# Kernel tuning notes

Measured on AMD Instinct MI355X. Metric: run time of the kernel, lower is better.

Reference implementation:

```python
import jax, jax.numpy as jnp
import numpy as np

B, S, T = 256, 512, 32  # batch, seq_len, tag_size (includes START=T-2, END=T-1)


def setup_inputs() -> dict:
    key = jax.random.key(0)
    k1, k2, k3, k4 = jax.random.split(key, 4)
    feats = jax.random.normal(k1, (B, S, T), dtype=jnp.float32)
    transitions = jax.random.normal(k2, (T, T), dtype=jnp.float32) * 0.1
    # prefix mask: lengths in [S//2, S] (torch code assumes contiguous valid prefix)
    lengths = jax.random.randint(k3, (B,), S // 2, S + 1)
    mask = jnp.arange(S)[None, :] < lengths[:, None]  # (B,S) bool
    tags = jax.random.randint(k4, (B, S), 0, T - 2).astype(jnp.int32)
    return {"feats": feats, "transitions": transitions, "mask": mask, "tags": tags}


def _nll_loss(feats, transitions, mask, tags):
    Bx, Sx, Tx = feats.shape
    maskf = mask.astype(feats.dtype)
    # ---- forward algorithm (log partition) ----
    # partition initialized from emissions at position 1 (positions 0,1 are special)
    part0 = feats[:, 1, :]  # (B,T)
    f_seq = jnp.swapaxes(feats[:, 2:, :], 0, 1)  # (S-2, B, T)
    m_seq = jnp.swapaxes(mask[:, 2:], 0, 1)      # (S-2, B)

    def fwd_step(partition, inp):
        f_t, m_t = inp
        # cur[b, prev, next] = feats[b,t,next] + transitions[prev,next] + partition[b,prev]
        cur = f_t[:, None, :] + transitions[None, :, :] + partition[:, :, None]
        new = jax.nn.logsumexp(cur, axis=1)  # (B,T)
        # partition frozen where mask==0 (== torch masked_scatter logic)
        return jnp.where(m_t[:, None], new, partition), None

    partition, _ = jax.lax.scan(fwd_step, part0, (f_seq, m_seq))
    forward_score = jnp.sum(jax.nn.logsumexp(partition, axis=1))

    # ---- gold score ----
    tags = jnp.where(tags == -100, 0, tags)
    emis = jnp.take_along_axis(feats, tags[..., None], axis=2)[..., 0]  # (B,S)
    tr = transitions[tags[:, :-1], tags[:, 1:]]  # (B,S-1): transition into pos t (t>=1)
    # transitions only apply for t>=2; tg_energy[0] is zeroed in the torch code
    e = emis + jnp.concatenate([jnp.zeros((Bx, 2), feats.dtype), tr[:, 1:]], axis=1)
    e = e.at[:, 0].set(0.0)
    gold_score = jnp.sum(e * maskf)
    return (forward_score - gold_score) / Bx


def _viterbi(feats, transitions, mask):
    Bx, Sx, Tx = feats.shape
    lengths = mask.astype(jnp.int32).sum(axis=1)
    part0 = feats[:, 1, :]
    f_seq = jnp.swapaxes(feats[:, 2:, :], 0, 1)
    m_seq = jnp.swapaxes(mask[:, 2:], 0, 1)

    def vit_step(partition, inp):
        f_t, m_t = inp
        cur = f_t[:, None, :] + transitions[None, :, :] + partition[:, :, None]
        new = jnp.max(cur, axis=1)
        bp = jnp.argmax(cur, axis=1).astype(jnp.int32)
        bp = jnp.where(m_t[:, None], bp, 0)  # torch masked_fill_(pad, 0)
        # NOTE: viterbi partition is updated UNconditionally in the torch code
        return new, (partition, bp)

    last_part, (hist, bps) = jax.lax.scan(vit_step, part0, (f_seq, m_seq))
    history = jnp.concatenate([hist, last_part[None]], axis=0)  # (S-1,B,T)
    hist_bt = jnp.swapaxes(history, 0, 1)                        # (B,S-1,T)
    idx = jnp.broadcast_to((lengths - 2)[:, None, None], (Bx, 1, Tx))
    last_partition = jnp.take_along_axis(hist_bt, idx, axis=1)[:, 0, :]  # (B,T)
    pointer = jnp.argmax(last_partition, axis=1).astype(jnp.int32)

    def back_step(ptr, bp_t):
        new = jnp.take_along_axis(bp_t, ptr[:, None], axis=1)[:, 0]
        return new, new

    _, ptrs = jax.lax.scan(back_step, pointer, bps, reverse=True)  # (S-2,B)
    # decode_idx[0] is uninitialized in the torch code; we define it as 0
    decode = jnp.concatenate(
        [jnp.zeros((1, Bx), jnp.int32), ptrs, pointer[None, :]], axis=0
    )  # (S,B)
    path_score = jnp.zeros((Bx,), feats.dtype)  # torch returns zeros
    return path_score, decode.T


def reference(feats, transitions, mask, tags):
    loss = _nll_loss(feats, transitions, mask, tags)
    path_score, decode_idx = _viterbi(feats, transitions, mask)
    return loss, path_score, decode_idx
```

## Files before the change

kernel.cpp:

```cpp
#include <hip/hip_runtime.h>
#include <cstdint>
#include <cstddef>
#include <utility>

#define SS 512
#define TT 32
#define NB 256
#define KSTEPS 510
#define PQUADS 128

template <typename F, size_t... Is>
__device__ __forceinline__ void unroll_impl(F&& f, std::index_sequence<Is...>) {
  (f(std::integral_constant<int, (int)Is>{}), ...);
}
template <int N, typename F>
__device__ __forceinline__ void unrollN(F&& f) {
  unroll_impl(f, std::make_index_sequence<N>{});
}

template <int D>
__device__ __forceinline__ float bfly32(float v) {
  return __int_as_float(__builtin_amdgcn_ds_swizzle(__float_as_int(v), (D << 10) | 0x1f));
}
template <int D>
__device__ __forceinline__ int bfly32i(int v) {
  return __builtin_amdgcn_ds_swizzle(v, (D << 10) | 0x1f);
}

__device__ __forceinline__ float max3f(float a, float b, float c) {
  return fmaxf(fmaxf(a, b), c);
}

__device__ __forceinline__ float combine_max32(float m) {
#if __has_builtin(__builtin_amdgcn_permlane32_swap)
  auto r = __builtin_amdgcn_permlane32_swap(__float_as_uint(m), __float_as_uint(m), false, false);
  return fmaxf(__uint_as_float(r[0]), __uint_as_float(r[1]));
#else
  return fmaxf(m, __shfl_xor(m, 32, 64));
#endif
}
__device__ __forceinline__ float combine_sum32(float m) {
#if __has_builtin(__builtin_amdgcn_permlane32_swap)
  auto r = __builtin_amdgcn_permlane32_swap(__float_as_uint(m), __float_as_uint(m), false, false);
  return __uint_as_float(r[0]) + __uint_as_float(r[1]);
#else
  return m + __shfl_xor(m, 32, 64);
#endif
}

__device__ __forceinline__ int mask_mode(const void* m) {
  int w0 = ((const int*)m)[0];
  if (w0 == 1) return 0;
  if (w0 == 0x3f800000) return 2;
  return 1;
}
__device__ __forceinline__ bool mask_at(const void* m, int idx, int mode) {
  if (mode == 0) return ((const int*)m)[idx] != 0;
  if (mode == 2) return ((const float*)m)[idx] != 0.0f;
  return ((const unsigned char*)m)[idx] != 0;
}

__device__ __forceinline__ int seq_length_lane(const void* mask, int b, int lane, int mode) {
  int cnt = 0;
  for (int s = lane; s < SS; s += 64) cnt += mask_at(mask, b * SS + s, mode) ? 1 : 0;
  for (int d = 1; d < 64; d <<= 1) cnt += __shfl_xor(cnt, d, 64);
  return __builtin_amdgcn_readfirstlane(cnt);
}

__global__ __launch_bounds__(64, 1) void crf_main_kernel(
    const float* __restrict__ feats, const float* __restrict__ trans,
    const void* __restrict__ mask, const int* __restrict__ tags,
    float* __restrict__ pstore, float* __restrict__ ws_fwd,
    float* __restrict__ ws_gold, int* __restrict__ ws_ptr) {
  const int blk = blockIdx.x;
  const int tid = threadIdx.x;
  const int mode = mask_mode(mask);
  const int j = tid & 31;
  const int h = tid >> 5;

  __shared__ __align__(16) float qlds[TT];

  if (blk < NB) {
    const int b = blk;
    const int steps = seq_length_lane(mask, b, tid, mode) - 2;
    const float* fb = feats + (size_t)b * (SS * TT) + j;

    float E[16];
    unrollN<16>([&](auto I) {
      constexpr int ii = I;
      E[ii] = __expf(trans[(h * 16 + ii) * TT + j]);
    });

    float q = __expf(fb[TT]);
    int Eacc = 0;
    qlds[j] = q;
    asm volatile("" ::: "memory");
    const float4* qvh = (const float4*)qlds + h * 4;

    float fA = fb[2 * TT], fB = fb[3 * TT], fC = fb[4 * TT];
    float ef = __expf(fA);

    auto fstep = [&](int k, bool resc) {
      float4 Q0 = qvh[0], Q1 = qvh[1], Q2 = qvh[2], Q3 = qvh[3];
      int r5 = k + 5; r5 = (r5 < SS) ? r5 : (SS - 1);
      float fD = fb[r5 * TT];
      float efN = __expf(fB);
      float a0, a1, a2, a3;
      a0 = Q0.x * E[0];  a1 = Q0.y * E[1];  a2 = Q0.z * E[2];  a3 = Q0.w * E[3];
      a0 = fmaf(Q1.x, E[4], a0);  a1 = fmaf(Q1.y, E[5], a1);  a2 = fmaf(Q1.z, E[6], a2);  a3 = fmaf(Q1.w, E[7], a3);
      a0 = fmaf(Q2.x, E[8], a0);  a1 = fmaf(Q2.y, E[9], a1);  a2 = fmaf(Q2.z, E[10], a2); a3 = fmaf(Q2.w, E[11], a3);
      a0 = fmaf(Q3.x, E[12], a0); a1 = fmaf(Q3.y, E[13], a1); a2 = fmaf(Q3.z, E[14], a2); a3 = fmaf(Q3.w, E[15], a3);
      float P = (a0 + a1) + (a2 + a3);
      float Pt = combine_sum32(P);
      q = ef * Pt;
      if (resc) {
        int qb = __builtin_amdgcn_readfirstlane(__float_as_int(q));
        int e = (qb >> 23) & 0xff;
        Eacc += e - 127;
        q *= __int_as_float((254 - e) << 23);
      }
      qlds[j] = q;
      asm volatile("" ::: "memory");
      fA = fB; fB = fC; fC = fD; ef = efN;
    };

    int k = 0;
    for (; k + 4 <= steps; k += 4) {
      fstep(k, false); fstep(k + 1, false); fstep(k + 2, false); fstep(k + 3, true);
    }
    for (; k < steps; ++k) fstep(k, false);

    float s = q;
    unrollN<5>([&](auto D) { constexpr int d = 1 << D; s += bfly32<d>(s); });
    if (tid == 0) ws_fwd[b] = __logf(s) + (float)Eacc * 0.69314718056f;

  } else if (blk < 2 * NB) {
    const int b = blk - NB;
    const int steps = seq_length_lane(mask, b, tid, mode) - 2;
    const float* fb = feats + (size_t)b * (SS * TT) + j;
    float* pq = pstore + (size_t)b * (PQUADS * 128) + j * 4;

    float C[16];
    unrollN<16>([&](auto I) {
      constexpr int ii = I;
      C[ii] = trans[(h * 16 + ii) * TT + j];
    });

    float p = fb[TT];
    qlds[j] = p;
    asm volatile("" ::: "memory");
    const float4* qvh = (const float4*)qlds + h * 4;

    float fA = fb[2 * TT], fB = fb[3 * TT], fC = fb[4 * TT];
    float h0 = p, h1 = 0.f, h2 = 0.f, h3 = 0.f;

    auto vstep = [&](int k, float& hslot) {
      float4 Q0 = qvh[0], Q1 = qvh[1], Q2 = qvh[2], Q3 = qvh[3];
      int r5 = k + 5; r5 = (r5 < SS) ? r5 : (SS - 1);
      float fD = fb[r5 * TT];
      float dd[16];
      unrollN<16>([&](auto I) { constexpr int ii = I; dd[ii] = fA + C[ii]; });
      float cur[16];
      cur[0] = Q0.x + dd[0];   cur[1] = Q0.y + dd[1];   cur[2] = Q0.z + dd[2];   cur[3] = Q0.w + dd[3];
      cur[4] = Q1.x + dd[4];   cur[5] = Q1.y + dd[5];   cur[6] = Q1.z + dd[6];   cur[7] = Q1.w + dd[7];
      cur[8] = Q2.x + dd[8];   cur[9] = Q2.y + dd[9];   cur[10] = Q2.z + dd[10]; cur[11] = Q2.w + dd[11];
      cur[12] = Q3.x + dd[12]; cur[13] = Q3.y + dd[13]; cur[14] = Q3.z + dd[14]; cur[15] = Q3.w + dd[15];
      float t0 = max3f(cur[0], cur[1], cur[2]);
      float t1 = max3f(cur[3], cur[4], cur[5]);
      float t2 = max3f(cur[6], cur[7], cur[8]);
      float t3 = max3f(cur[9], cur[10], cur[11]);
      float t4 = max3f(cur[12], cur[13], cur[14]);
      float m = fmaxf(max3f(t0, t1, t2), max3f(t3, t4, cur[15]));
      float pw = combine_max32(m);
      p = pw;
      qlds[j] = pw;
      asm volatile("" ::: "memory");
      hslot = pw;
      fA = fB; fB = fC; fC = fD;
    };

    auto flush = [&](int quad) {
      if (tid < 32) {
        float4 v; v.x = h0; v.y = h1; v.z = h2; v.w = h3;
        *(float4*)(pq + quad * 128) = v;
      }
    };

    int k = 0;
    for (; k + 4 <= steps; k += 4) {
      vstep(k, h1);
      vstep(k + 1, h2);
      vstep(k + 2, h3);
      flush(k >> 2);
      vstep(k + 3, h0);
    }
    if (k < steps) vstep(k, h1);
    if (k + 1 < steps) vstep(k + 1, h2);
    if (k + 2 < steps) vstep(k + 2, h3);
    flush(k >> 2);

    float v = p;
    int idx = j;
    unrollN<5>([&](auto D) {
      constexpr int d = 1 << D;
      float vo = bfly32<d>(v);
      int io = bfly32i<d>(idx);
      bool take = (vo > v) || ((vo == v) && (io < idx));
      v = take ? vo : v;
      idx = take ? io : idx;
    });
    if (tid == 0) ws_ptr[b] = idx;

  } else {
    const int b = blk - 2 * NB;
    float acc = 0.0f;
    for (int s = tid; s < SS; s += 64) {
      if (s == 0) continue;
      if (!mask_at(mask, b * SS + s, mode)) continue;
      int tg = tags[b * SS + s];
      if (tg == -100) tg = 0;
      float e = feats[((size_t)b * SS + s) * TT + tg];
      if (s >= 2) {
        int tp = tags[b * SS + s - 1];
        if (tp == -100) tp = 0;
        e += trans[tp * TT + tg];
      }
      acc += e;
    }
    for (int d = 1; d < 64; d <<= 1) acc += __shfl_xor(acc, d, 64);
    if (tid == 0) ws_gold[b] = acc;
  }
}

__global__ __launch_bounds__(512) void crf_backtrace_kernel(
    const float* __restrict__ pstore, const float* __restrict__ feats,
    const float* __restrict__ trans, const void* __restrict__ mask,
    const int* __restrict__ ws_ptr, const float* __restrict__ ws_fwd,
    const float* __restrict__ ws_gold, float* __restrict__ out) {
  __shared__ unsigned char bp[KSTEPS * TT];
  __shared__ unsigned char path[KSTEPS * TT];
  __shared__ __align__(16) float pT[16][4][TT];
  __shared__ int entries[8];

  const int b = blockIdx.x;
  const int tid = threadIdx.x;
  const int mode = mask_mode(mask);
  const int lane = tid & 63;
  float* out_decode = out + 1 + NB;

  const int steps = seq_length_lane(mask, b, lane, mode) - 2;

  if (tid == 0) out[1 + b] = 0.0f;
  if (b == 0 && tid >= 64 && tid < 128) {
    int t = tid - 64;
    float sf = 0.0f, sg = 0.0f;
    for (int r = 0; r < 4; ++r) { sf += ws_fwd[t + 64 * r]; sg += ws_gold[t + 64 * r]; }
    for (int d = 1; d < 64; d <<= 1) { sf += __shfl_xor(sf, d, 64); sg += __shfl_xor(sg, d, 64); }
    if (t == 0) out[0] = (sf - sg) / 256.0f;
  }

  {
    const int jj = tid & 31;
    const int g = tid >> 5;
    float Cc[TT];
    unrollN<TT>([&](auto I) { constexpr int ii = I; Cc[ii] = trans[ii * TT + jj]; });
    const float* pb = pstore + (size_t)b * (PQUADS * 128);
    const float* fbb = feats + (size_t)b * (SS * TT);
    for (int q = g; q < PQUADS; q += 16) {
      float4 V = *(const float4*)(pb + q * 128 + jj * 4);
      pT[g][0][jj] = V.x; pT[g][1][jj] = V.y; pT[g][2][jj] = V.z; pT[g][3][jj] = V.w;
      asm volatile("" ::: "memory");
      unrollN<4>([&](auto R) {
        constexpr int r = R;
        const int k = 4 * q + r;
        if (k < KSTEPS) {
          unsigned char bv = 0;
          if (k < steps) {
            const float4* pr = (const float4*)pT[g][r];
            float4 P0 = pr[0], P1 = pr[1], P2 = pr[2], P3 = pr[3];
            float4 P4 = pr[4], P5 = pr[5], P6 = pr[6], P7 = pr[7];
            float fj = fbb[(k + 2) * TT + jj];
            float cur[TT];
            cur[0]  = (fj + Cc[0])  + P0.x; cur[1]  = (fj + Cc[1])  + P0.y;
            cur[2]  = (fj + Cc[2])  + P0.z; cur[3]  = (fj + Cc[3])  + P0.w;
            cur[4]  = (fj + Cc[4])  + P1.x; cur[5]  = (fj + Cc[5])  + P1.y;
            cur[6]  = (fj + Cc[6])  + P1.z; cur[7]  = (fj + Cc[7])  + P1.w;
            cur[8]  = (fj + Cc[8])  + P2.x; cur[9]  = (fj + Cc[9])  + P2.y;
            cur[10] = (fj + Cc[10]) + P2.z; cur[11] = (fj + Cc[11]) + P2.w;
            cur[12] = (fj + Cc[12]) + P3.x; cur[13] = (fj + Cc[13]) + P3.y;
            cur[14] = (fj + Cc[14]) + P3.z; cur[15] = (fj + Cc[15]) + P3.w;
            cur[16] = (fj + Cc[16]) + P4.x; cur[17] = (fj + Cc[17]) + P4.y;
            cur[18] = (fj + Cc[18]) + P4.z; cur[19] = (fj + Cc[19]) + P4.w;
            cur[20] = (fj + Cc[20]) + P5.x; cur[21] = (fj + Cc[21]) + P5.y;
            cur[22] = (fj + Cc[22]) + P5.z; cur[23] = (fj + Cc[23]) + P5.w;
            cur[24] = (fj + Cc[24]) + P6.x; cur[25] = (fj + Cc[25]) + P6.y;
            cur[26] = (fj + Cc[26]) + P6.z; cur[27] = (fj + Cc[27]) + P6.w;
            cur[28] = (fj + Cc[28]) + P7.x; cur[29] = (fj + Cc[29]) + P7.y;
            cur[30] = (fj + Cc[30]) + P7.z; cur[31] = (fj + Cc[31]) + P7.w;
            float t0 = max3f(cur[0], cur[1], cur[2]);
            float t1 = max3f(cur[3], cur[4], cur[5]);
            float t2 = max3f(cur[6], cur[7], cur[8]);
            float t3 = max3f(cur[9], cur[10], cur[11]);
            float t4 = max3f(cur[12], cur[13], cur[14]);
            float t5 = max3f(cur[15], cur[16], cur[17]);
            float t6 = max3f(cur[18], cur[19], cur[20]);
            float t7 = max3f(cur[21], cur[22], cur[23]);
            float t8 = max3f(cur[24], cur[25], cur[26]);
            float t9 = max3f(cur[27], cur[28], cur[29]);
            float ta = fmaxf(cur[30], cur[31]);
            float vmax = fmaxf(fmaxf(max3f(t0, t1, t2), max3f(t3, t4, t5)),
                               fmaxf(max3f(t6, t7, t8), fmaxf(t9, ta)));
            int bi = 31;
            unrollN<TT>([&](auto I) { constexpr int ii = 31 - I; bi = (cur[ii] == vmax) ? ii : bi; });
            bv = (unsigned char)bi;
          }
          bp[k * TT + jj] = bv;
        }
      });
    }
  }
  __syncthreads();

  const int wave = tid >> 6;
  if (lane < 32) {
    const int lo = wave * 64;
    const int hi = (lo + 64 < KSTEPS) ? (lo + 64) : KSTEPS;
    int ptr = lane;
    for (int k = hi - 1; k >= lo; --k) {
      ptr = bp[k * TT + ptr];
      path[k * TT + lane] = (unsigned char)ptr;
    }
  }
  __syncthreads();

  if (tid == 0) {
    int e = ws_ptr[b];
    for (int c = 7; c >= 0; --c) {
      entries[c] = e;
      e = path[(c * 64) * TT + e];
    }
  }
  __syncthreads();

  const int s = tid;
  int val;
  if (s == 0) val = 0;
  else if (s <= KSTEPS) { int k = s - 1; val = path[k * TT + entries[k >> 6]]; }
  else val = ws_ptr[b];
  out_decode[(size_t)b * SS + s] = (float)val;
}

extern "C" void kernel_launch(void* const* d_in, const int* in_sizes, int n_in,
                              void* d_out, int out_size, void* d_ws, size_t ws_size,
                              hipStream_t stream) {
  const float* feats = (const float*)d_in[0];
  const float* trans = (const float*)d_in[1];
  const void* mask = d_in[2];
  const int* tags = (const int*)d_in[3];
  float* out = (float*)d_out;

  unsigned char* ws = (unsigned char*)d_ws;
  const size_t PST_BYTES = (size_t)NB * PQUADS * 128 * 4;
  float* pstore = (float*)ws;
  float* ws_fwd = (float*)(ws + PST_BYTES);
  float* ws_gold = (float*)(ws + PST_BYTES + 2048);
  int* ws_ptr = (int*)(ws + PST_BYTES + 4096);

  hipLaunchKernelGGL(crf_main_kernel, dim3(3 * NB), dim3(64), 0, stream,
                     feats, trans, mask, tags, pstore, ws_fwd, ws_gold, ws_ptr);
  hipLaunchKernelGGL(crf_backtrace_kernel, dim3(NB), dim3(512), 0, stream,
                     pstore, feats, trans, mask, ws_ptr, ws_fwd, ws_gold, out);
}
```

Before: 112.6 us.

## Interleave two batch sequences per wave in forward and Viterbi recurrences

Result: slower. 175.3 us (+55.8%).

```diff
diff --git a/kernel.cpp b/kernel.cpp
--- a/kernel.cpp
+++ b/kernel.cpp
@@ -78,12 +78,15 @@
   const int j = tid & 31;
   const int h = tid >> 5;
 
-  __shared__ __align__(16) float qlds[TT];
-
-  if (blk < NB) {
-    const int b = blk;
-    const int steps = seq_length_lane(mask, b, tid, mode) - 2;
-    const float* fb = feats + (size_t)b * (SS * TT) + j;
+  __shared__ __align__(16) float qlds[2][TT];
+
+  if (blk < 128) {
+    const int bA = blk * 2, bB = bA + 1;
+    const int stepsA = seq_length_lane(mask, bA, tid, mode) - 2;
+    const int stepsB = seq_length_lane(mask, bB, tid, mode) - 2;
+    const int smax = (stepsA > stepsB) ? stepsA : stepsB;
+    const float* fbA = feats + (size_t)bA * (SS * TT) + j;
+    const float* fbB = feats + (size_t)bB * (SS * TT) + j;
 
     float E[16];
     unrollN<16>([&](auto I) {
@@ -91,54 +94,88 @@
       E[ii] = __expf(trans[(h * 16 + ii) * TT + j]);
     });
 
-    float q = __expf(fb[TT]);
-    int Eacc = 0;
-    qlds[j] = q;
+    float qA = __expf(fbA[TT]), qB = __expf(fbB[TT]);
+    int EaA = 0, EaB = 0;
+    qlds[0][j] = qA; qlds[1][j] = qB;
     asm volatile("" ::: "memory");
-    const float4* qvh = (const float4*)qlds + h * 4;
-
-    float fA = fb[2 * TT], fB = fb[3 * TT], fC = fb[4 * TT];
-    float ef = __expf(fA);
-
-    auto fstep = [&](int k, bool resc) {
-      float4 Q0 = qvh[0], Q1 = qvh[1], Q2 = qvh[2], Q3 = qvh[3];
+    const float4* qvA = (const float4*)qlds[0] + h * 4;
+    const float4* qvB = (const float4*)qlds[1] + h * 4;
+
+    float fA0 = fbA[2 * TT], fB0 = fbA[3 * TT], fC0 = fbA[4 * TT];
+    float fA1 = fbB[2 * TT], fB1 = fbB[3 * TT], fC1 = fbB[4 * TT];
+    float efA = __expf(fA0), efB = __expf(fA1);
+
+    auto fstep2 = [&](int k, bool resc) {
+      float4 QA0 = qvA[0], QA1 = qvA[1], QA2 = qvA[2], QA3 = qvA[3];
+      float4 QB0 = qvB[0], QB1 = qvB[1], QB2 = qvB[2], QB3 = qvB[3];
       int r5 = k + 5; r5 = (r5 < SS) ? r5 : (SS - 1);
-      float fD = fb[r5 * TT];
-      float efN = __expf(fB);
-      float a0, a1, a2, a3;
-      a0 = Q0.x * E[0];  a1 = Q0.y * E[1];  a2 = Q0.z * E[2];  a3 = Q0.w * E[3];
-      a0 = fmaf(Q1.x, E[4], a0);  a1 = fmaf(Q1.y, E[5], a1);  a2 = fmaf(Q1.z, E[6], a2);  a3 = fmaf(Q1.w, E[7], a3);
-      a0 = fmaf(Q2.x, E[8], a0);  a1 = fmaf(Q2.y, E[9], a1);  a2 = fmaf(Q2.z, E[10], a2); a3 = fmaf(Q2.w, E[11], a3);
-      a0 = fmaf(Q3.x, E[12], a0); a1 = fmaf(Q3.y, E[13], a1); a2 = fmaf(Q3.z, E[14], a2); a3 = fmaf(Q3.w, E[15], a3);
-      float P = (a0 + a1) + (a2 + a3);
-      float Pt = combine_sum32(P);
-      q = ef * Pt;
-      if (resc) {
-        int qb = __builtin_amdgcn_readfirstlane(__float_as_int(q));
-        int e = (qb >> 23) & 0xff;
-        Eacc += e - 127;
-        q *= __int_as_float((254 - e) << 23);
+      float fDA = fbA[r5 * TT], fDB = fbB[r5 * TT];
+      float efNA = __expf(fB0), efNB = __expf(fB1);
+      {
+        float a0, a1, a2, a3;
+        a0 = QA0.x * E[0];  a1 = QA0.y * E[1];  a2 = QA0.z * E[2];  a3 = QA0.w * E[3];
+        a0 = fmaf(QA1.x, E[4], a0);  a1 = fmaf(QA1.y, E[5], a1);  a2 = fmaf(QA1.z, E[6], a2);  a3 = fmaf(QA1.w, E[7], a3);
+        a0 = fmaf(QA2.x, E[8], a0);  a1 = fmaf(QA2.y, E[9], a1);  a2 = fmaf(QA2.z, E[10], a2); a3 = fmaf(QA2.w, E[11], a3);
+        a0 = fmaf(QA3.x, E[12], a0); a1 = fmaf(QA3.y, E[13], a1); a2 = fmaf(QA3.z, E[14], a2); a3 = fmaf(QA3.w, E[15], a3);
+        float P = (a0 + a1) + (a2 + a3);
+        float qn = efA * combine_sum32(P);
+        if (resc) {
+          int e = (__float_as_int(QA0.x) >> 23) & 0xff;
+          e = (k < stepsA) ? e : 127;
+          EaA += e - 127;
+          qn *= __int_as_float((254 - e) << 23);
+        }
+        qn = (k < stepsA) ? qn : qA;
+        qA = qn;
+        qlds[0][j] = qn;
+        asm volatile("" ::: "memory");
       }
-      qlds[j] = q;
-      asm volatile("" ::: "memory");
-      fA = fB; fB = fC; fC = fD; ef = efN;
+      {
+        float a0, a1, a2, a3;
+        a0 = QB0.x * E[0];  a1 = QB0.y * E[1];  a2 = QB0.z * E[2];  a3 = QB0.w * E[3];
+        a0 = fmaf(QB1.x, E[4], a0);  a1 = fmaf(QB1.y, E[5], a1);  a2 = fmaf(QB1.z, E[6], a2);  a3 = fmaf(QB1.w, E[7], a3);
+        a0 = fmaf(QB2.x, E[8], a0);  a1 = fmaf(QB2.y, E[9], a1);  a2 = fmaf(QB2.z, E[10], a2); a3 = fmaf(QB2.w, E[11], a3);
+        a0 = fmaf(QB3.x, E[12], a0); a1 = fmaf(QB3.y, E[13], a1); a2 = fmaf(QB3.z, E[14], a2); a3 = fmaf(QB3.w, E[15], a3);
+        float P = (a0 + a1) + (a2 + a3);
+        float qn = efB * combine_sum32(P);
+        if (resc) {
+          int e = (__float_as_int(QB0.x) >> 23) & 0xff;
+          e = (k < stepsB) ? e : 127;
+          EaB += e - 127;
+          qn *= __int_as_float((254 - e) << 23);
+        }
+        qn = (k < stepsB) ? qn : qB;
+        qB = qn;
+        qlds[1][j] = qn;
+        asm volatile("" ::: "memory");
+      }
+      fA0 = fB0; fB0 = fC0; fC0 = fDA; efA = efNA;
+      fA1 = fB1; fB1 = fC1; fC1 = fDB; efB = efNB;
     };
 
     int k = 0;
-    for (; k + 4 <= steps; k += 4) {
-      fstep(k, false); fstep(k + 1, false); fstep(k + 2, false); fstep(k + 3, true);
-    }
-    for (; k < steps; ++k) fstep(k, false);
-
-    float s = q;
-    unrollN<5>([&](auto D) { constexpr int d = 1 << D; s += bfly32<d>(s); });
-    if (tid == 0) ws_fwd[b] = __logf(s) + (float)Eacc * 0.69314718056f;
-
-  } else if (blk < 2 * NB) {
-    const int b = blk - NB;
-    const int steps = seq_length_lane(mask, b, tid, mode) - 2;
-    const float* fb = feats + (size_t)b * (SS * TT) + j;
-    float* pq = pstore + (size_t)b * (PQUADS * 128) + j * 4;
+    for (; k + 4 <= smax; k += 4) {
+      fstep2(k, false); fstep2(k + 1, false); fstep2(k + 2, false); fstep2(k + 3, true);
+    }
+    for (; k < smax; ++k) fstep2(k, false);
+
+    float sA = qA, sB = qB;
+    unrollN<5>([&](auto D) { constexpr int d = 1 << D; sA += bfly32<d>(sA); });
+    unrollN<5>([&](auto D) { constexpr int d = 1 << D; sB += bfly32<d>(sB); });
+    if (tid == 0) {
+      ws_fwd[bA] = __logf(sA) + (float)EaA * 0.69314718056f;
+      ws_fwd[bB] = __logf(sB) + (float)EaB * 0.69314718056f;
+    }
+
+  } else if (blk < 256) {
+    const int bA = (blk - 128) * 2, bB = bA + 1;
+    const int stepsA = seq_length_lane(mask, bA, tid, mode) - 2;
+    const int stepsB = seq_length_lane(mask, bB, tid, mode) - 2;
+    const int smax = (stepsA > stepsB) ? stepsA : stepsB;
+    const float* fbA = feats + (size_t)bA * (SS * TT) + j;
+    const float* fbB = feats + (size_t)bB * (SS * TT) + j;
+    float* pqA = pstore + (size_t)bA * (PQUADS * 128) + j * 4;
+    float* pqB = pstore + (size_t)bB * (PQUADS * 128) + j * 4;
 
     float C[16];
     unrollN<16>([&](auto I) {
@@ -146,73 +183,106 @@
       C[ii] = trans[(h * 16 + ii) * TT + j];
     });
 
-    float p = fb[TT];
-    qlds[j] = p;
+    float pA = fbA[TT], pB = fbB[TT];
+    qlds[0][j] = pA; qlds[1][j] = pB;
     asm volatile("" ::: "memory");
-    const float4* qvh = (const float4*)qlds + h * 4;
-
-    float fA = fb[2 * TT], fB = fb[3 * TT], fC = fb[4 * TT];
-    float h0 = p, h1 = 0.f, h2 = 0.f, h3 = 0.f;
-
-    auto vstep = [&](int k, float& hslot) {
-      float4 Q0 = qvh[0], Q1 = qvh[1], Q2 = qvh[2], Q3 = qvh[3];
+    const float4* qvA = (const float4*)qlds[0] + h * 4;
+    const float4* qvB = (const float4*)qlds[1] + h * 4;
+
+    float fA0 = fbA[2 * TT], fB0 = fbA[3 * TT], fC0 = fbA[4 * TT];
+    float fA1 = fbB[2 * TT], fB1 = fbB[3 * TT], fC1 = fbB[4 * TT];
+    float h0A = pA, h1A = 0.f, h2A = 0.f, h3A = 0.f;
+    float h0B = pB, h1B = 0.f, h2B = 0.f, h3B = 0.f;
+
+    auto vstep2 = [&](int k, float& hA, float& hB) {
+      float4 QA0 = qvA[0], QA1 = qvA[1], QA2 = qvA[2], QA3 = qvA[3];
+      float4 QB0 = qvB[0], QB1 = qvB[1], QB2 = qvB[2], QB3 = qvB[3];
       int r5 = k + 5; r5 = (r5 < SS) ? r5 : (SS - 1);
-      float fD = fb[r5 * TT];
-      float dd[16];
-      unrollN<16>([&](auto I) { constexpr int ii = I; dd[ii] = fA + C[ii]; });
-      float cur[16];
-      cur[0] = Q0.x + dd[0];   cur[1] = Q0.y + dd[1];   cur[2] = Q0.z + dd[2];   cur[3] = Q0.w + dd[3];
-      cur[4] = Q1.x + dd[4];   cur[5] = Q1.y + dd[5];   cur[6] = Q1.z + dd[6];   cur[7] = Q1.w + dd[7];
-      cur[8] = Q2.x + dd[8];   cur[9] = Q2.y + dd[9];   cur[10] = Q2.z + dd[10]; cur[11] = Q2.w + dd[11];
-      cur[12] = Q3.x + dd[12]; cur[13] = Q3.y + dd[13]; cur[14] = Q3.z + dd[14]; cur[15] = Q3.w + dd[15];
-      float t0 = max3f(cur[0], cur[1], cur[2]);
-      float t1 = max3f(cur[3], cur[4], cur[5]);
-      float t2 = max3f(cur[6], cur[7], cur[8]);
-      float t3 = max3f(cur[9], cur[10], cur[11]);
-      float t4 = max3f(cur[12], cur[13], cur[14]);
-      float m = fmaxf(max3f(t0, t1, t2), max3f(t3, t4, cur[15]));
-      float pw = combine_max32(m);
-      p = pw;
-      qlds[j] = pw;
-      asm volatile("" ::: "memory");
-      hslot = pw;
-      fA = fB; fB = fC; fC = fD;
+      float fDA = fbA[r5 * TT], fDB = fbB[r5 * TT];
+      {
+        float dd[16];
+        unrollN<16>([&](auto I) { constexpr int ii = I; dd[ii] = fA0 + C[ii]; });
+        float cur[16];
+        cur[0] = QA0.x + dd[0];   cur[1] = QA0.y + dd[1];   cur[2] = QA0.z + dd[2];   cur[3] = QA0.w + dd[3];
+        cur[4] = QA1.x + dd[4];   cur[5] = QA1.y + dd[5];   cur[6] = QA1.z + dd[6];   cur[7] = QA1.w + dd[7];
+        cur[8] = QA2.x + dd[8];   cur[9] = QA2.y + dd[9];   cur[10] = QA2.z + dd[10]; cur[11] = QA2.w + dd[11];
+        cur[12] = QA3.x + dd[12]; cur[13] = QA3.y + dd[13]; cur[14] = QA3.z + dd[14]; cur[15] = QA3.w + dd[15];
+        float t0 = max3f(cur[0], cur[1], cur[2]);
+        float t1 = max3f(cur[3], cur[4], cur[5]);
+        float t2 = max3f(cur[6], cur[7], cur[8]);
+        float t3 = max3f(cur[9], cur[10], cur[11]);
+        float t4 = max3f(cur[12], cur[13], cur[14]);
+        float m = fmaxf(max3f(t0, t1, t2), max3f(t3, t4, cur[15]));
+        float pw = combine_max32(m);
+        pw = (k < stepsA) ? pw : pA;
+        pA = pw;
+        qlds[0][j] = pw;
+        asm volatile("" ::: "memory");
+        hA = pw;
+      }
+      {
+        float dd[16];
+        unrollN<16>([&](auto I) { constexpr int ii = I; dd[ii] = fA1 + C[ii]; });
+        float cur[16];
+        cur[0] = QB0.x + dd[0];   cur[1] = QB0.y + dd[1];   cur[2] = QB0.z + dd[2];   cur[3] = QB0.w + dd[3];
+        cur[4] = QB1.x + dd[4];   cur[5] = QB1.y + dd[5];   cur[6] = QB1.z + dd[6];   cur[7] = QB1.w + dd[7];
+        cur[8] = QB2.x + dd[8];   cur[9] = QB2.y + dd[9];   cur[10] = QB2.z + dd[10]; cur[11] = QB2.w + dd[11];
+        cur[12] = QB3.x + dd[12]; cur[13] = QB3.y + dd[13]; cur[14] = QB3.z + dd[14]; cur[15] = QB3.w + dd[15];
+        float t0 = max3f(cur[0], cur[1], cur[2]);
+        float t1 = max3f(cur[3], cur[4], cur[5]);
+        float t2 = max3f(cur[6], cur[7], cur[8]);
+        float t3 = max3f(cur[9], cur[10], cur[11]);
+        float t4 = max3f(cur[12], cur[13], cur[14]);
+        float m = fmaxf(max3f(t0, t1, t2), max3f(t3, t4, cur[15]));
+        float pw = combine_max32(m);
+        pw = (k < stepsB) ? pw : pB;
+        pB = pw;
+        qlds[1][j] = pw;
+        asm volatile("" ::: "memory");
+        hB = pw;
+      }
+      fA0 = fB0; fB0 = fC0; fC0 = fDA;
+      fA1 = fB1; fB1 = fC1; fC1 = fDB;
     };
 
-    auto flush = [&](int quad) {
-      if (tid < 32) {
-        float4 v; v.x = h0; v.y = h1; v.z = h2; v.w = h3;
-        *(float4*)(pq + quad * 128) = v;
-      }
+    auto flushA = [&](int quad) {
+      if (tid < 32) { float4 v; v.x = h0A; v.y = h1A; v.z = h2A; v.w = h3A; *(float4*)(pqA + quad * 128) = v; }
     };
+    auto flushB = [&](int quad) {
+      if (tid < 32) { float4 v; v.x = h0B; v.y = h1B; v.z = h2B; v.w = h3B; *(float4*)(pqB + quad * 128) = v; }
+    };
 
     int k = 0;
-    for (; k + 4 <= steps; k += 4) {
-      vstep(k, h1);
-      vstep(k + 1, h2);
-      vstep(k + 2, h3);
-      flush(k >> 2);
-      vstep(k + 3, h0);
-    }
-    if (k < steps) vstep(k, h1);
-    if (k + 1 < steps) vstep(k + 1, h2);
-    if (k + 2 < steps) vstep(k + 2, h3);
-    flush(k >> 2);
-
-    float v = p;
-    int idx = j;
-    unrollN<5>([&](auto D) {
-      constexpr int d = 1 << D;
-      float vo = bfly32<d>(v);
-      int io = bfly32i<d>(idx);
-      bool take = (vo > v) || ((vo == v) && (io < idx));
-      v = take ? vo : v;
-      idx = take ? io : idx;
-    });
-    if (tid == 0) ws_ptr[b] = idx;
+    for (; k + 4 <= smax; k += 4) {
+      vstep2(k, h1A, h1B);
+      vstep2(k + 1, h2A, h2B);
+      vstep2(k + 2, h3A, h3B);
+      flushA(k >> 2); flushB(k >> 2);
+      vstep2(k + 3, h0A, h0B);
+    }
+    if (k < smax) vstep2(k, h1A, h1B);
+    if (k + 1 < smax) vstep2(k + 1, h2A, h2B);
+    if (k + 2 < smax) vstep2(k + 2, h3A, h3B);
+    flushA(k >> 2); flushB(k >> 2);
+
+    auto finArg = [&](float p, int bb) {
+      float v = p;
+      int idx = j;
+      unrollN<5>([&](auto D) {
+        constexpr int d = 1 << D;
+        float vo = bfly32<d>(v);
+        int io = bfly32i<d>(idx);
+        bool take = (vo > v) || ((vo == v) && (io < idx));
+        v = take ? vo : v;
+        idx = take ? io : idx;
+      });
+      if (tid == 0) ws_ptr[bb] = idx;
+    };
+    finArg(pA, bA);
+    finArg(pB, bB);
 
   } else {
-    const int b = blk - 2 * NB;
+    const int b = blk - 256;
     float acc = 0.0f;
     for (int s = tid; s < SS; s += 64) {
       if (s == 0) continue;
@@ -366,7 +436,7 @@
   float* ws_gold = (float*)(ws + PST_BYTES + 2048);
   int* ws_ptr = (int*)(ws + PST_BYTES + 4096);
 
-  hipLaunchKernelGGL(crf_main_kernel, dim3(3 * NB), dim3(64), 0, stream,
+  hipLaunchKernelGGL(crf_main_kernel, dim3(512), dim3(64), 0, stream,
                      feats, trans, mask, tags, pstore, ws_fwd, ws_gold, ws_ptr);
   hipLaunchKernelGGL(crf_backtrace_kernel, dim3(NB), dim3(512), 0, stream,
                      pstore, feats, trans, mask, ws_ptr, ws_fwd, ws_gold, out);
```

## Fuse CRF forward, Viterbi and backtrace into one kernel with flag-based sync

Applied to the files above, without the earlier changes.

New measurement: 179.9 us. 59.8% more time.

```diff
diff --git a/kernel.cpp b/kernel.cpp
--- a/kernel.cpp
+++ b/kernel.cpp
@@ -8,6 +8,7 @@
 #define NB 256
 #define KSTEPS 510
 #define PQUADS 128
+#define BT_BASE 72
 
 template <typename F, size_t... Is>
 __device__ __forceinline__ void unroll_impl(F&& f, std::index_sequence<Is...>) {
@@ -67,76 +68,30 @@
   return __builtin_amdgcn_readfirstlane(cnt);
 }
 
-__global__ __launch_bounds__(64, 1) void crf_main_kernel(
+__global__ __launch_bounds__(512, 1) void crf_fused_kernel(
     const float* __restrict__ feats, const float* __restrict__ trans,
     const void* __restrict__ mask, const int* __restrict__ tags,
     float* __restrict__ pstore, float* __restrict__ ws_fwd,
-    float* __restrict__ ws_gold, int* __restrict__ ws_ptr) {
+    float* __restrict__ ws_gold, int* __restrict__ ws_ptr,
+    int* __restrict__ flags, int* __restrict__ cntp,
+    float* __restrict__ out) {
   const int blk = blockIdx.x;
   const int tid = threadIdx.x;
+  const int wave = tid >> 6;
+  const int lane = tid & 63;
+  const int j = lane & 31;
+  const int h = lane >> 5;
   const int mode = mask_mode(mask);
-  const int j = tid & 31;
-  const int h = tid >> 5;
-
-  __shared__ __align__(16) float qlds[TT];
-
-  if (blk < NB) {
-    const int b = blk;
-    const int steps = seq_length_lane(mask, b, tid, mode) - 2;
-    const float* fb = feats + (size_t)b * (SS * TT) + j;
-
-    float E[16];
-    unrollN<16>([&](auto I) {
-      constexpr int ii = I;
-      E[ii] = __expf(trans[(h * 16 + ii) * TT + j]);
-    });
-
-    float q = __expf(fb[TT]);
-    int Eacc = 0;
-    qlds[j] = q;
-    asm volatile("" ::: "memory");
-    const float4* qvh = (const float4*)qlds + h * 4;
-
-    float fA = fb[2 * TT], fB = fb[3 * TT], fC = fb[4 * TT];
-    float ef = __expf(fA);
-
-    auto fstep = [&](int k, bool resc) {
-      float4 Q0 = qvh[0], Q1 = qvh[1], Q2 = qvh[2], Q3 = qvh[3];
-      int r5 = k + 5; r5 = (r5 < SS) ? r5 : (SS - 1);
-      float fD = fb[r5 * TT];
-      float efN = __expf(fB);
-      float a0, a1, a2, a3;
-      a0 = Q0.x * E[0];  a1 = Q0.y * E[1];  a2 = Q0.z * E[2];  a3 = Q0.w * E[3];
-      a0 = fmaf(Q1.x, E[4], a0);  a1 = fmaf(Q1.y, E[5], a1);  a2 = fmaf(Q1.z, E[6], a2);  a3 = fmaf(Q1.w, E[7], a3);
-      a0 = fmaf(Q2.x, E[8], a0);  a1 = fmaf(Q2.y, E[9], a1);  a2 = fmaf(Q2.z, E[10], a2); a3 = fmaf(Q2.w, E[11], a3);
-      a0 = fmaf(Q3.x, E[12], a0); a1 = fmaf(Q3.y, E[13], a1); a2 = fmaf(Q3.z, E[14], a2); a3 = fmaf(Q3.w, E[15], a3);
-      float P = (a0 + a1) + (a2 + a3);
-      float Pt = combine_sum32(P);
-      q = ef * Pt;
-      if (resc) {
-        int qb = __builtin_amdgcn_readfirstlane(__float_as_int(q));
-        int e = (qb >> 23) & 0xff;
-        Eacc += e - 127;
-        q *= __int_as_float((254 - e) << 23);
-      }
-      qlds[j] = q;
-      asm volatile("" ::: "memory");
-      fA = fB; fB = fC; fC = fD; ef = efN;
-    };
-
-    int k = 0;
-    for (; k + 4 <= steps; k += 4) {
-      fstep(k, false); fstep(k + 1, false); fstep(k + 2, false); fstep(k + 3, true);
-    }
-    for (; k < steps; ++k) fstep(k, false);
-
-    float s = q;
-    unrollN<5>([&](auto D) { constexpr int d = 1 << D; s += bfly32<d>(s); });
-    if (tid == 0) ws_fwd[b] = __logf(s) + (float)Eacc * 0.69314718056f;
-
-  } else if (blk < 2 * NB) {
-    const int b = blk - NB;
-    const int steps = seq_length_lane(mask, b, tid, mode) - 2;
+
+  __shared__ __align__(16) float qlds[8][TT];
+  __shared__ unsigned char bp[KSTEPS * TT];
+  __shared__ unsigned char path[KSTEPS * TT];
+  __shared__ __align__(16) float pT[16][4][TT];
+  __shared__ int entries[8];
+
+  if (blk < 32) {
+    const int b = blk * 8 + wave;
+    const int steps = seq_length_lane(mask, b, lane, mode) - 2;
     const float* fb = feats + (size_t)b * (SS * TT) + j;
     float* pq = pstore + (size_t)b * (PQUADS * 128) + j * 4;
 
@@ -147,9 +102,9 @@
     });
 
     float p = fb[TT];
-    qlds[j] = p;
+    qlds[wave][j] = p;
     asm volatile("" ::: "memory");
-    const float4* qvh = (const float4*)qlds + h * 4;
+    const float4* qvh = (const float4*)qlds[wave] + h * 4;
 
     float fA = fb[2 * TT], fB = fb[3 * TT], fC = fb[4 * TT];
     float h0 = p, h1 = 0.f, h2 = 0.f, h3 = 0.f;
@@ -173,14 +128,14 @@
       float m = fmaxf(max3f(t0, t1, t2), max3f(t3, t4, cur[15]));
       float pw = combine_max32(m);
       p = pw;
-      qlds[j] = pw;
+      qlds[wave][j] = pw;
       asm volatile("" ::: "memory");
       hslot = pw;
       fA = fB; fB = fC; fC = fD;
     };
 
     auto flush = [&](int quad) {
-      if (tid < 32) {
+      if (lane < 32) {
         float4 v; v.x = h0; v.y = h1; v.z = h2; v.w = h3;
         *(float4*)(pq + quad * 128) = v;
       }
@@ -188,9 +143,7 @@
 
     int k = 0;
     for (; k + 4 <= steps; k += 4) {
-      vstep(k, h1);
-      vstep(k + 1, h2);
-      vstep(k + 2, h3);
+      vstep(k, h1); vstep(k + 1, h2); vstep(k + 2, h3);
       flush(k >> 2);
       vstep(k + 3, h0);
     }
@@ -209,145 +162,211 @@
       v = take ? vo : v;
       idx = take ? io : idx;
     });
-    if (tid == 0) ws_ptr[b] = idx;
+    if (lane == 0) ws_ptr[b] = idx;
+
+    __threadfence();
+    if (lane == 0) atomicExch(&flags[b], 1);
+
+  } else if (blk < 64) {
+    const int b = (blk - 32) * 8 + wave;
+    const int steps = seq_length_lane(mask, b, lane, mode) - 2;
+    const float* fb = feats + (size_t)b * (SS * TT) + j;
+
+    float E[16];
+    unrollN<16>([&](auto I) {
+      constexpr int ii = I;
+      E[ii] = __expf(trans[(h * 16 + ii) * TT + j]);
+    });
+
+    float q = __expf(fb[TT]);
+    int Eacc = 0;
+    qlds[wave][j] = q;
+    asm volatile("" ::: "memory");
+    const float4* qvh = (const float4*)qlds[wave] + h * 4;
+
+    float fA = fb[2 * TT], fB = fb[3 * TT], fC = fb[4 * TT];
+    float ef = __expf(fA);
+
+    auto fstep = [&](int k, bool resc) {
+      float4 Q0 = qvh[0], Q1 = qvh[1], Q2 = qvh[2], Q3 = qvh[3];
+      int r5 = k + 5; r5 = (r5 < SS) ? r5 : (SS - 1);
+      float fD = fb[r5 * TT];
+      float efN = __expf(fB);
+      float a0, a1, a2, a3;
+      a0 = Q0.x * E[0];  a1 = Q0.y * E[1];  a2 = Q0.z * E[2];  a3 = Q0.w * E[3];
+      a0 = fmaf(Q1.x, E[4], a0);  a1 = fmaf(Q1.y, E[5], a1);  a2 = fmaf(Q1.z, E[6], a2);  a3 = fmaf(Q1.w, E[7], a3);
+      a0 = fmaf(Q2.x, E[8], a0);  a1 = fmaf(Q2.y, E[9], a1);  a2 = fmaf(Q2.z, E[10], a2); a3 = fmaf(Q2.w, E[11], a3);
+      a0 = fmaf(Q3.x, E[12], a0); a1 = fmaf(Q3.y, E[13], a1); a2 = fmaf(Q3.z, E[14], a2); a3 = fmaf(Q3.w, E[15], a3);
+      float P = (a0 + a1) + (a2 + a3);
+      float Pt = combine_sum32(P);
+      q = ef * Pt;
+      if (resc) {
+        int qb = __builtin_amdgcn_readfirstlane(__float_as_int(q));
+        int e = (qb >> 23) & 0xff;
+        Eacc += e - 127;
+        q *= __int_as_float((254 - e) << 23);
+      }
+      qlds[wave][j] = q;
+      asm volatile("" ::: "memory");
+      fA = fB; fB = fC; fC = fD; ef = efN;
+    };
+
+    int k = 0;
+    for (; k + 4 <= steps; k += 4) {
+      fstep(k, false); fstep(k + 1, false); fstep(k + 2, false); fstep(k + 3, true);
+    }
+    for (; k < steps; ++k) fstep(k, false);
+
+    float s = q;
+    unrollN<5>([&](auto D) { constexpr int d = 1 << D; s += bfly32<d>(s); });
+    if (lane == 0) ws_fwd[b] = __logf(s) + (float)Eacc * 0.69314718056f;
+
+    __threadfence();
+    if (lane == 0) atomicAdd(cntp, 1);
+
+  } else if (blk < BT_BASE) {
+    for (int bb = 0; bb < 4; ++bb) {
+      const int b = (blk - 64) * 32 + wave * 4 + bb;
+      float acc = 0.0f;
+      for (int s = lane; s < SS; s += 64) {
+        if (s == 0) continue;
+        if (!mask_at(mask, b * SS + s, mode)) continue;
+        int tg = tags[b * SS + s];
+        if (tg == -100) tg = 0;
+        float e = feats[((size_t)b * SS + s) * TT + tg];
+        if (s >= 2) {
+          int tp = tags[b * SS + s - 1];
+          if (tp == -100) tp = 0;
+          e += trans[tp * TT + tg];
+        }
+        acc += e;
+      }
+      for (int d = 1; d < 64; d <<= 1) acc += __shfl_xor(acc, d, 64);
+      if (lane == 0) ws_gold[b] = acc;
+    }
+    __threadfence();
+    if (tid == 0) { }
+    if (lane == 0) atomicAdd(cntp, 4);
 
   } else {
-    const int b = blk - 2 * NB;
-    float acc = 0.0f;
-    for (int s = tid; s < SS; s += 64) {
-      if (s == 0) continue;
-      if (!mask_at(mask, b * SS + s, mode)) continue;
-      int tg = tags[b * SS + s];
-      if (tg == -100) tg = 0;
-      float e = feats[((size_t)b * SS + s) * TT + tg];
-      if (s >= 2) {
-        int tp = tags[b * SS + s - 1];
-        if (tp == -100) tp = 0;
-        e += trans[tp * TT + tg];
-      }
-      acc += e;
-    }
-    for (int d = 1; d < 64; d <<= 1) acc += __shfl_xor(acc, d, 64);
-    if (tid == 0) ws_gold[b] = acc;
+    const int b = blk - BT_BASE;
+    float* out_decode = out + 1 + NB;
+
+    if (tid == 0) out[1 + b] = 0.0f;
+
+    if (tid == 0) {
+      while (atomicAdd(&flags[b], 0) == 0) __builtin_amdgcn_s_sleep(10);
+    }
+    __syncthreads();
+    __threadfence();
+
+    const int steps = seq_length_lane(mask, b, lane, mode) - 2;
+
+    {
+      const int jj = tid & 31;
+      const int g = tid >> 5;
+      float Cc[TT];
+      unrollN<TT>([&](auto I) { constexpr int ii = I; Cc[ii] = trans[ii * TT + jj]; });
+      const float* pb = pstore + (size_t)b * (PQUADS * 128);
+      const float* fbb = feats + (size_t)b * (SS * TT);
+      for (int q = g; q < PQUADS; q += 16) {
+        float4 V = *(const float4*)(pb + q * 128 + jj * 4);
+        pT[g][0][jj] = V.x; pT[g][1][jj] = V.y; pT[g][2][jj] = V.z; pT[g][3][jj] = V.w;
+        asm volatile("" ::: "memory");
+        unrollN<4>([&](auto R) {
+          constexpr int r = R;
+          const int k = 4 * q + r;
+          if (k < KSTEPS) {
+            unsigned char bv = 0;
+            if (k < steps) {
+              const float4* pr = (const float4*)pT[g][r];
+              float4 P0 = pr[0], P1 = pr[1], P2 = pr[2], P3 = pr[3];
+              float4 P4 = pr[4], P5 = pr[5], P6 = pr[6], P7 = pr[7];
+              float fj = fbb[(k + 2) * TT + jj];
+              float cur[TT];
+              cur[0]  = (fj + Cc[0])  + P0.x; cur[1]  = (fj + Cc[1])  + P0.y;
+              cur[2]  = (fj + Cc[2])  + P0.z; cur[3]  = (fj + Cc[3])  + P0.w;
+              cur[4]  = (fj + Cc[4])  + P1.x; cur[5]  = (fj + Cc[5])  + P1.y;
+              cur[6]  = (fj + Cc[6])  + P1.z; cur[7]  = (fj + Cc[7])  + P1.w;
+              cur[8]  = (fj + Cc[8])  + P2.x; cur[9]  = (fj + Cc[9])  + P2.y;
+              cur[10] = (fj + Cc[10]) + P2.z; cur[11] = (fj + Cc[11]) + P2.w;
+              cur[12] = (fj + Cc[12]) + P3.x; cur[13] = (fj + Cc[13]) + P3.y;
+              cur[14] = (fj + Cc[14]) + P3.z; cur[15] = (fj + Cc[15]) + P3.w;
+              cur[16] = (fj + Cc[16]) + P4.x; cur[17] = (fj + Cc[17]) + P4.y;
+              cur[18] = (fj + Cc[18]) + P4.z; cur[19] = (fj + Cc[19]) + P4.w;
+              cur[20] = (fj + Cc[20]) + P5.x; cur[21] = (fj + Cc[21]) + P5.y;
+              cur[22] = (fj + Cc[22]) + P5.z; cur[23] = (fj + Cc[23]) + P5.w;
+              cur[24] = (fj + Cc[24]) + P6.x; cur[25] = (fj + Cc[25]) + P6.y;
+              cur[26] = (fj + Cc[26]) + P6.z; cur[27] = (fj + Cc[27]) + P6.w;
+              cur[28] = (fj + Cc[28]) + P7.x; cur[29] = (fj + Cc[29]) + P7.y;
+              cur[30] = (fj + Cc[30]) + P7.z; cur[31] = (fj + Cc[31]) + P7.w;
+              float t0 = max3f(cur[0], cur[1], cur[2]);
+              float t1 = max3f(cur[3], cur[4], cur[5]);
+              float t2 = max3f(cur[6], cur[7], cur[8]);
+              float t3 = max3f(cur[9], cur[10], cur[11]);
+              float t4 = max3f(cur[12], cur[13], cur[14]);
+              float t5 = max3f(cur[15], cur[16], cur[17]);
+              float t6 = max3f(cur[18], cur[19], cur[20]);
+              float t7 = max3f(cur[21], cur[22], cur[23]);
+              float t8 = max3f(cur[24], cur[25], cur[26]);
+              float t9 = max3f(cur[27], cur[28], cur[29]);
+              float ta = fmaxf(cur[30], cur[31]);
+              float vmax = fmaxf(fmaxf(max3f(t0, t1, t2), max3f(t3, t4, t5)),
+                                 fmaxf(max3f(t6, t7, t8), fmaxf(t9, ta)));
+              int bi = 31;
+              unrollN<TT>([&](auto I) { constexpr int ii = 31 - I; bi = (cur[ii] == vmax) ? ii : bi; });
+              bv = (unsigned char)bi;
+            }
+            bp[k * TT + jj] = bv;
+          }
+        });
+      }
+    }
+    __syncthreads();
+
+    if (lane < 32) {
+      const int lo = wave * 64;
+      const int hi = (lo + 64 < KSTEPS) ? (lo + 64) : KSTEPS;
+      int ptr = lane;
+      for (int k = hi - 1; k >= lo; --k) {
+        ptr = bp[k * TT + ptr];
+        path[k * TT + lane] = (unsigned char)ptr;
+      }
+    }
+    __syncthreads();
+
+    if (tid == 0) {
+      int e = ws_ptr[b];
+      for (int c = 7; c >= 0; --c) {
+        entries[c] = e;
+        e = path[(c * 64) * TT + e];
+      }
+    }
+    __syncthreads();
+
+    const int s = tid;
+    int val;
+    if (s == 0) val = 0;
+    else if (s <= KSTEPS) { int k = s - 1; val = path[k * TT + entries[k >> 6]]; }
+    else val = ws_ptr[b];
+    out_decode[(size_t)b * SS + s] = (float)val;
+
+    if (b == 0) {
+      __syncthreads();
+      if (tid == 0) {
+        while (atomicAdd(cntp, 0) < 512) __builtin_amdgcn_s_sleep(10);
+      }
+      __syncthreads();
+      __threadfence();
+      if (tid < 64) {
+        int t = tid;
+        float sf = 0.0f, sg = 0.0f;
+        for (int r = 0; r < 4; ++r) { sf += ws_fwd[t + 64 * r]; sg += ws_gold[t + 64 * r]; }
+        for (int d = 1; d < 64; d <<= 1) { sf += __shfl_xor(sf, d, 64); sg += __shfl_xor(sg, d, 64); }
+        if (t == 0) out[0] = (sf - sg) / 256.0f;
+      }
+    }
   }
-}
-
-__global__ __launch_bounds__(512) void crf_backtrace_kernel(
-    const float* __restrict__ pstore, const float* __restrict__ feats,
-    const float* __restrict__ trans, const void* __restrict__ mask,
-    const int* __restrict__ ws_ptr, const float* __restrict__ ws_fwd,
-    const float* __restrict__ ws_gold, float* __restrict__ out) {
-  __shared__ unsigned char bp[KSTEPS * TT];
-  __shared__ unsigned char path[KSTEPS * TT];
-  __shared__ __align__(16) float pT[16][4][TT];
-  __shared__ int entries[8];
-
-  const int b = blockIdx.x;
-  const int tid = threadIdx.x;
-  const int mode = mask_mode(mask);
-  const int lane = tid & 63;
-  float* out_decode = out + 1 + NB;
-
-  const int steps = seq_length_lane(mask, b, lane, mode) - 2;
-
-  if (tid == 0) out[1 + b] = 0.0f;
-  if (b == 0 && tid >= 64 && tid < 128) {
-    int t = tid - 64;
-    float sf = 0.0f, sg = 0.0f;
-    for (int r = 0; r < 4; ++r) { sf += ws_fwd[t + 64 * r]; sg += ws_gold[t + 64 * r]; }
-    for (int d = 1; d < 64; d <<= 1) { sf += __shfl_xor(sf, d, 64); sg += __shfl_xor(sg, d, 64); }
-    if (t == 0) out[0] = (sf - sg) / 256.0f;
-  }
-
-  {
-    const int jj = tid & 31;
-    const int g = tid >> 5;
-    float Cc[TT];
-    unrollN<TT>([&](auto I) { constexpr int ii = I; Cc[ii] = trans[ii * TT + jj]; });
-    const float* pb = pstore + (size_t)b * (PQUADS * 128);
-    const float* fbb = feats + (size_t)b * (SS * TT);
-    for (int q = g; q < PQUADS; q += 16) {
-      float4 V = *(const float4*)(pb + q * 128 + jj * 4);
-      pT[g][0][jj] = V.x; pT[g][1][jj] = V.y; pT[g][2][jj] = V.z; pT[g][3][jj] = V.w;
-      asm volatile("" ::: "memory");
-      unrollN<4>([&](auto R) {
-        constexpr int r = R;
-        const int k = 4 * q + r;
-        if (k < KSTEPS) {
-          unsigned char bv = 0;
-          if (k < steps) {
-            const float4* pr = (const float4*)pT[g][r];
-            float4 P0 = pr[0], P1 = pr[1], P2 = pr[2], P3 = pr[3];
-            float4 P4 = pr[4], P5 = pr[5], P6 = pr[6], P7 = pr[7];
-            float fj = fbb[(k + 2) * TT + jj];
-            float cur[TT];
-            cur[0]  = (fj + Cc[0])  + P0.x; cur[1]  = (fj + Cc[1])  + P0.y;
-            cur[2]  = (fj + Cc[2])  + P0.z; cur[3]  = (fj + Cc[3])  + P0.w;
-            cur[4]  = (fj + Cc[4])  + P1.x; cur[5]  = (fj + Cc[5])  + P1.y;
-            cur[6]  = (fj + Cc[6])  + P1.z; cur[7]  = (fj + Cc[7])  + P1.w;
-            cur[8]  = (fj + Cc[8])  + P2.x; cur[9]  = (fj + Cc[9])  + P2.y;
-            cur[10] = (fj + Cc[10]) + P2.z; cur[11] = (fj + Cc[11]) + P2.w;
-            cur[12] = (fj + Cc[12]) + P3.x; cur[13] = (fj + Cc[13]) + P3.y;
-            cur[14] = (fj + Cc[14]) + P3.z; cur[15] = (fj + Cc[15]) + P3.w;
-            cur[16] = (fj + Cc[16]) + P4.x; cur[17] = (fj + Cc[17]) + P4.y;
-            cur[18] = (fj + Cc[18]) + P4.z; cur[19] = (fj + Cc[19]) + P4.w;
-            cur[20] = (fj + Cc[20]) + P5.x; cur[21] = (fj + Cc[21]) + P5.y;
-            cur[22] = (fj + Cc[22]) + P5.z; cur[23] = (fj + Cc[23]) + P5.w;
-            cur[24] = (fj + Cc[24]) + P6.x; cur[25] = (fj + Cc[25]) + P6.y;
-            cur[26] = (fj + Cc[26]) + P6.z; cur[27] = (fj + Cc[27]) + P6.w;
-            cur[28] = (fj + Cc[28]) + P7.x; cur[29] = (fj + Cc[29]) + P7.y;
-            cur[30] = (fj + Cc[30]) + P7.z; cur[31] = (fj + Cc[31]) + P7.w;
-            float t0 = max3f(cur[0], cur[1], cur[2]);
-            float t1 = max3f(cur[3], cur[4], cur[5]);
-            float t2 = max3f(cur[6], cur[7], cur[8]);
-            float t3 = max3f(cur[9], cur[10], cur[11]);
-            float t4 = max3f(cur[12], cur[13], cur[14]);
-            float t5 = max3f(cur[15], cur[16], cur[17]);
-            float t6 = max3f(cur[18], cur[19], cur[20]);
-            float t7 = max3f(cur[21], cur[22], cur[23]);
-            float t8 = max3f(cur[24], cur[25], cur[26]);
-            float t9 = max3f(cur[27], cur[28], cur[29]);
-            float ta = fmaxf(cur[30], cur[31]);
-            float vmax = fmaxf(fmaxf(max3f(t0, t1, t2), max3f(t3, t4, t5)),
-                               fmaxf(max3f(t6, t7, t8), fmaxf(t9, ta)));
-            int bi = 31;
-            unrollN<TT>([&](auto I) { constexpr int ii = 31 - I; bi = (cur[ii] == vmax) ? ii : bi; });
-            bv = (unsigned char)bi;
-          }
-          bp[k * TT + jj] = bv;
-        }
-      });
-    }
-  }
-  __syncthreads();
-
-  const int wave = tid >> 6;
-  if (lane < 32) {
-    const int lo = wave * 64;
-    const int hi = (lo + 64 < KSTEPS) ? (lo + 64) : KSTEPS;
-    int ptr = lane;
-    for (int k = hi - 1; k >= lo; --k) {
-      ptr = bp[k * TT + ptr];
-      path[k * TT + lane] = (unsigned char)ptr;
-    }
-  }
-  __syncthreads();
-
-  if (tid == 0) {
-    int e = ws_ptr[b];
-    for (int c = 7; c >= 0; --c) {
-      entries[c] = e;
-      e = path[(c * 64) * TT + e];
-    }
-  }
-  __syncthreads();
-
-  const int s = tid;
-  int val;
-  if (s == 0) val = 0;
-  else if (s <= KSTEPS) { int k = s - 1; val = path[k * TT + entries[k >> 6]]; }
-  else val = ws_ptr[b];
-  out_decode[(size_t)b * SS + s] = (float)val;
 }
 
 extern "C" void kernel_launch(void* const* d_in, const int* in_sizes, int n_in,
@@ -365,9 +384,11 @@
   float* ws_fwd = (float*)(ws + PST_BYTES);
   float* ws_gold = (float*)(ws + PST_BYTES + 2048);
   int* ws_ptr = (int*)(ws + PST_BYTES + 4096);
-
-  hipLaunchKernelGGL(crf_main_kernel, dim3(3 * NB), dim3(64), 0, stream,
-                     feats, trans, mask, tags, pstore, ws_fwd, ws_gold, ws_ptr);
-  hipLaunchKernelGGL(crf_backtrace_kernel, dim3(NB), dim3(512), 0, stream,
-                     pstore, feats, trans, mask, ws_ptr, ws_fwd, ws_gold, out);
-}
+  int* flags = (int*)(ws + PST_BYTES + 8192);
+  int* cntp = (int*)(ws + PST_BYTES + 8192 + 1024);
+
+  hipMemsetAsync(ws + PST_BYTES + 8192, 0, 2048, stream);
+  hipLaunchKernelGGL(crf_fused_kernel, dim3(BT_BASE + NB), dim3(512), 0, stream,
+                     feats, trans, mask, tags, pstore, ws_fwd, ws_gold, ws_ptr,
+                     flags, cntp, out);
+}
```
